# Optimization experiments

Measured on AMD Instinct MI355X. Metric: run time of the kernel, lower is better.

## Reference

```python
import jax, jax.numpy as jnp
import numpy as np


def setup_inputs() -> dict:
    key = jax.random.key(0)
    k1, k2 = jax.random.split(key)
    token_inputs = jax.random.normal(k1, (4, 2048, 4096), dtype=jnp.float32)
    w_gate = jax.random.normal(k2, (4096, 64), dtype=jnp.float32)
    return {"token_inputs": token_inputs, "w_gate": w_gate, "expert_capacity": 40}


def reference(token_inputs, w_gate, expert_capacity):
    # Gating: [b, n, d] @ [d, e] -> [b, n, e]
    router_logits = jnp.einsum('bnd,de->bne', token_inputs, w_gate)

    # Router z-loss: mean of squared logsumexp over experts.
    z_loss = jnp.mean(jax.nn.logsumexp(router_logits, axis=-1) ** 2)

    router_probs = jax.nn.softmax(router_logits, axis=-1)
    num_experts = router_probs.shape[-1]

    # Top-1 (Switch) routing.
    expert_index = jnp.argmax(router_probs, axis=-1)          # [b, n]
    expert_gate = jnp.max(router_probs, axis=-1)              # [b, n]
    expert_mask = jax.nn.one_hot(expert_index, num_experts,
                                 dtype=router_probs.dtype)    # [b, n, e]

    # Load-balancing auxiliary loss.
    density = jnp.mean(expert_mask, axis=1)                   # [b, e] dispatch fraction
    density_proxy = jnp.mean(router_probs, axis=1)            # [b, e] mean prob
    aux_loss = jnp.mean(density * density_proxy) * (num_experts ** 2)

    # Capacity assignment via cumulative sum over tokens (0-based slot index).
    position_in_expert = (jnp.cumsum(expert_mask, axis=1) - 1.0) * expert_mask  # [b, n, e]
    within_capacity = (position_in_expert < expert_capacity).astype(router_probs.dtype) * expert_mask

    pos_idx = position_in_expert.astype(jnp.int32)            # [b, n, e]
    # Dispatch: one-hot over capacity slots, zeroed for dropped tokens. [b, n, e, c]
    dispatch_tensor = within_capacity[..., None] * jax.nn.one_hot(
        pos_idx, expert_capacity, dtype=router_probs.dtype)
    # Combine: dispatch scaled by the router gate probability.
    combine_tensor = dispatch_tensor * expert_gate[:, :, None, None]

    return dispatch_tensor, combine_tensor, aux_loss, z_loss
```

## Files before the change

kernel.cpp:

```cpp
#include <hip/hip_runtime.h>
#include <stdint.h>

#define B_    4
#define N_    2048
#define D_    4096
#define E_    64
#define TOKENS (B_ * N_)
#define KT    16
#define TM    128
#define KS    16
#define KCHUNK (D_ / KS)
#define NIT   (KCHUNK / KT)
#define PA    (TM + 4)
#define PW    (E_ + 4)

typedef float vfloat4 __attribute__((ext_vector_type(4)));

__global__ __launch_bounds__(256) void k_gemm_z(const float* __restrict__ A,
                                                const float* __restrict__ W,
                                                float* __restrict__ P,
                                                float* __restrict__ out,
                                                float* __restrict__ probsum,
                                                float* __restrict__ losses) {
    __shared__ float As[KT][PA];
    __shared__ float Ws[KT][PW];

    const int tid   = threadIdx.x;
    const int tok0  = blockIdx.x * TM;
    const int kc    = blockIdx.y;
    const int kbase = kc * KCHUNK;
    const int blin  = kc * gridDim.x + blockIdx.x;

    const int t0 = (tid & 15) * 8;
    const int e0 = (tid >> 4) * 4;

    const int a_k = (tid & 3) * 4;
    const int a_t = tid >> 2;
    const int w_k = tid >> 4;
    const int w_e = (tid & 15) * 4;

    vfloat4* zbase = reinterpret_cast<vfloat4*>(out) + (size_t)blin * 10240 + tid;
    int zstep = 0;
    const vfloat4 z4 = {0.f, 0.f, 0.f, 0.f};

    if (blin == 0) {
        probsum[tid] = 0.f;
        if (tid < 2) losses[tid] = 0.f;
    }

    const float* gA = A + (size_t)tok0 * D_ + kbase;

    float4 pa0 = *reinterpret_cast<const float4*>(gA + (size_t)a_t * D_ + a_k);
    float4 pa1 = *reinterpret_cast<const float4*>(gA + (size_t)(a_t + 64) * D_ + a_k);
    float4 pw  = *reinterpret_cast<const float4*>(W + (size_t)(kbase + w_k) * E_ + w_e);

    float acc[8][4] = {{0.f}};

    #pragma unroll 1
    for (int it = 0; it < NIT; ++it) {
        As[a_k + 0][a_t]      = pa0.x;
        As[a_k + 1][a_t]      = pa0.y;
        As[a_k + 2][a_t]      = pa0.z;
        As[a_k + 3][a_t]      = pa0.w;
        As[a_k + 0][a_t + 64] = pa1.x;
        As[a_k + 1][a_t + 64] = pa1.y;
        As[a_k + 2][a_t + 64] = pa1.z;
        As[a_k + 3][a_t + 64] = pa1.w;
        *reinterpret_cast<float4*>(&Ws[w_k][w_e]) = pw;
        __syncthreads();

        if (it + 1 < NIT) {
            const int ko = (it + 1) * KT;
            pa0 = *reinterpret_cast<const float4*>(gA + (size_t)a_t * D_ + ko + a_k);
            pa1 = *reinterpret_cast<const float4*>(gA + (size_t)(a_t + 64) * D_ + ko + a_k);
            pw  = *reinterpret_cast<const float4*>(W + (size_t)(kbase + ko + w_k) * E_ + w_e);
        }

        {
            const int nz = (it < 8) ? 3 : 2;
            for (int j = 0; j < nz; ++j) {
                __builtin_nontemporal_store(z4, zbase + (size_t)zstep * 256);
                ++zstep;
            }
        }

        #pragma unroll
        for (int kk = 0; kk < KT; ++kk) {
            float a[8], b[4];
            *reinterpret_cast<float4*>(&a[0]) = *reinterpret_cast<const float4*>(&As[kk][t0]);
            *reinterpret_cast<float4*>(&a[4]) = *reinterpret_cast<const float4*>(&As[kk][t0 + 4]);
            *reinterpret_cast<float4*>(&b[0]) = *reinterpret_cast<const float4*>(&Ws[kk][e0]);
            #pragma unroll
            for (int i = 0; i < 8; ++i)
                #pragma unroll
                for (int j = 0; j < 4; ++j)
                    acc[i][j] += a[i] * b[j];
        }
        __syncthreads();
    }

    float* base = P + ((size_t)kc * TOKENS + tok0) * E_;
    #pragma unroll
    for (int i = 0; i < 8; ++i) {
        const float4 v = make_float4(acc[i][0], acc[i][1], acc[i][2], acc[i][3]);
        *reinterpret_cast<float4*>(&base[(size_t)(t0 + i) * E_ + e0]) = v;
    }
}

__global__ __launch_bounds__(256) void k_softmax(const float* __restrict__ P,
                                                 int* __restrict__ idx,
                                                 float* __restrict__ gate,
                                                 float* __restrict__ probsum,
                                                 float* __restrict__ out_z) {
    const int tid  = threadIdx.x;
    const int wid  = tid >> 6;
    const int lane = tid & 63;
    const int tok  = blockIdx.x * 4 + wid;

    float l = 0.f;
    #pragma unroll
    for (int kc = 0; kc < KS; ++kc)
        l += P[((size_t)kc * TOKENS + tok) * E_ + lane];

    float m = l; int mi = lane;
    #pragma unroll
    for (int off = 32; off > 0; off >>= 1) {
        const float om = __shfl_down(m, off);
        const int   oi = __shfl_down(mi, off);
        if (om > m || (om == m && oi < mi)) { m = om; mi = oi; }
    }
    m  = __shfl(m, 0);
    mi = __shfl(mi, 0);

    const float p = __expf(l - m);
    float s = p;
    #pragma unroll
    for (int off = 32; off > 0; off >>= 1) s += __shfl_down(s, off);
    s = __shfl(s, 0);

    __shared__ float pacc[4][E_];
    __shared__ float zv[4];
    pacc[wid][lane] = p / s;
    if (lane == 0) {
        const float lse = m + logf(s);
        zv[wid]   = lse * lse;
        idx[tok]  = mi;
        gate[tok] = 1.0f / s;
    }
    __syncthreads();

    if (tid < E_) {
        const float ps = pacc[0][tid] + pacc[1][tid] + pacc[2][tid] + pacc[3][tid];
        const int b = (blockIdx.x * 4) / N_;
        atomicAdd(&probsum[b * E_ + tid], ps);
    }
    if (tid == 0)
        atomicAdd(out_z, (zv[0] + zv[1] + zv[2] + zv[3]) * (1.0f / (float)TOKENS));
}

__global__ __launch_bounds__(64) void k_posloss(const int* __restrict__ idx,
                                                const float* __restrict__ gate,
                                                const float* __restrict__ probsum,
                                                float* __restrict__ out,
                                                float* __restrict__ out_aux,
                                                int C, size_t half) {
    const int b = blockIdx.x >> 6;
    const int e = blockIdx.x & 63;
    const int lane = threadIdx.x;
    const int*   ib = idx  + b * N_;
    const float* gb = gate + b * N_;
    float* ob = out + (size_t)b * N_ * E_ * C;

    int running = 0;
    for (int step = 0; step < N_ / 64; ++step) {
        const int t = step * 64 + lane;
        const bool match = (ib[t] == e);
        const unsigned long long mask = __ballot(match);
        if (match) {
            const int p = running + __popcll(mask & ((1ull << lane) - 1ull));
            if (p < C) {
                const size_t off = (size_t)t * E_ * C + (size_t)e * C + p;
                ob[off] = 1.0f;
                ob[half + off] = gb[t];
            }
        }
        running += __popcll(mask);
    }
    if (lane == 0)
        atomicAdd(out_aux,
                  (float)running * probsum[b * E_ + e] * (1.0f / 262144.0f));
}

extern "C" void kernel_launch(void* const* d_in, const int* in_sizes, int n_in,
                              void* d_out, int out_size, void* d_ws, size_t ws_size,
                              hipStream_t stream) {
    const float* A = (const float*)d_in[0];
    const float* W = (const float*)d_in[1];
    float* out = (float*)d_out;

    const size_t half = ((size_t)out_size - 2) / 2;
    const int C = (int)(half / ((size_t)TOKENS * E_));

    float* P = (float*)d_ws;
    size_t off = (size_t)KS * TOKENS * E_;
    int*   idx     = (int*)(P + off);   off += TOKENS;
    float* gate    = P + off;           off += TOKENS;
    float* probsum = P + off;           off += B_ * E_;

    float* out_aux = out + 2 * half;
    float* out_z   = out + 2 * half + 1;

    k_gemm_z<<<dim3(TOKENS / TM, KS), 256, 0, stream>>>(A, W, P, out, probsum,
                                                        out_aux);
    k_softmax<<<TOKENS / 4, 256, 0, stream>>>(P, idx, gate, probsum, out_z);
    k_posloss<<<B_ * E_, 64, 0, stream>>>(idx, gate, probsum, out, out_aux, C, half);
}
```

Baseline: 339.0 us.

## Split output zero-fill into dedicated blocks and transpose GEMM thread tile

The zero-fill of the large dispatch/combine output moves out of the GEMM main loop into 256 dedicated fill blocks launched in the same 1D grid, with the GEMM blocks re-indexed after them. The per-thread GEMM micro-tile also changes from 8 tokens x 4 experts to 4 tokens x 8 experts, which alters the LDS read pattern. The aim is to stop interleaving stores with the compute loop so fill and GEMM blocks run concurrently. The trade-off is that fill blocks are scheduled first and may delay GEMM blocks. Correctness relies on qsteps dividing the output size exactly.

```diff
diff --git a/kernel.cpp b/kernel.cpp
--- a/kernel.cpp
+++ b/kernel.cpp
@@ -13,6 +13,8 @@
 #define NIT   (KCHUNK / KT)
 #define PA    (TM + 4)
 #define PW    (E_ + 4)
+#define FILLB 256
+#define GEMMB ((TOKENS / TM) * KS)
 
 typedef float vfloat4 __attribute__((ext_vector_type(4)));
 
@@ -21,40 +23,46 @@
                                                 float* __restrict__ P,
                                                 float* __restrict__ out,
                                                 float* __restrict__ probsum,
-                                                float* __restrict__ losses) {
+                                                float* __restrict__ losses,
+                                                int qsteps) {
+    const int tid = threadIdx.x;
+
+    if (blockIdx.x < FILLB) {
+        vfloat4* zb = reinterpret_cast<vfloat4*>(out)
+                    + (size_t)blockIdx.x * (size_t)qsteps * 256 + tid;
+        const vfloat4 z4 = {0.f, 0.f, 0.f, 0.f};
+        for (int s = 0; s < qsteps; ++s)
+            __builtin_nontemporal_store(z4, zb + (size_t)s * 256);
+        if (blockIdx.x == 0) {
+            probsum[tid] = 0.f;
+            if (tid < 2) losses[tid] = 0.f;
+        }
+        return;
+    }
+
     __shared__ float As[KT][PA];
     __shared__ float Ws[KT][PW];
 
-    const int tid   = threadIdx.x;
-    const int tok0  = blockIdx.x * TM;
-    const int kc    = blockIdx.y;
+    const int bid   = blockIdx.x - FILLB;
+    const int tok0  = (bid & 63) * TM;
+    const int kc    = bid >> 6;
     const int kbase = kc * KCHUNK;
-    const int blin  = kc * gridDim.x + blockIdx.x;
-
-    const int t0 = (tid & 15) * 8;
-    const int e0 = (tid >> 4) * 4;
+
+    const int t0 = (tid & 31) * 4;
+    const int e0 = (tid >> 5) * 8;
 
     const int a_k = (tid & 3) * 4;
     const int a_t = tid >> 2;
     const int w_k = tid >> 4;
     const int w_e = (tid & 15) * 4;
 
-    vfloat4* zbase = reinterpret_cast<vfloat4*>(out) + (size_t)blin * 10240 + tid;
-    int zstep = 0;
-    const vfloat4 z4 = {0.f, 0.f, 0.f, 0.f};
-
-    if (blin == 0) {
-        probsum[tid] = 0.f;
-        if (tid < 2) losses[tid] = 0.f;
-    }
-
     const float* gA = A + (size_t)tok0 * D_ + kbase;
 
     float4 pa0 = *reinterpret_cast<const float4*>(gA + (size_t)a_t * D_ + a_k);
     float4 pa1 = *reinterpret_cast<const float4*>(gA + (size_t)(a_t + 64) * D_ + a_k);
     float4 pw  = *reinterpret_cast<const float4*>(W + (size_t)(kbase + w_k) * E_ + w_e);
 
-    float acc[8][4] = {{0.f}};
+    float acc[4][8] = {{0.f}};
 
     #pragma unroll 1
     for (int it = 0; it < NIT; ++it) {
@@ -76,24 +84,16 @@
             pw  = *reinterpret_cast<const float4*>(W + (size_t)(kbase + ko + w_k) * E_ + w_e);
         }
 
-        {
-            const int nz = (it < 8) ? 3 : 2;
-            for (int j = 0; j < nz; ++j) {
-                __builtin_nontemporal_store(z4, zbase + (size_t)zstep * 256);
-                ++zstep;
-            }
-        }
-
         #pragma unroll
         for (int kk = 0; kk < KT; ++kk) {
-            float a[8], b[4];
+            float a[4], b[8];
             *reinterpret_cast<float4*>(&a[0]) = *reinterpret_cast<const float4*>(&As[kk][t0]);
-            *reinterpret_cast<float4*>(&a[4]) = *reinterpret_cast<const float4*>(&As[kk][t0 + 4]);
             *reinterpret_cast<float4*>(&b[0]) = *reinterpret_cast<const float4*>(&Ws[kk][e0]);
+            *reinterpret_cast<float4*>(&b[4]) = *reinterpret_cast<const float4*>(&Ws[kk][e0 + 4]);
             #pragma unroll
-            for (int i = 0; i < 8; ++i)
+            for (int i = 0; i < 4; ++i)
                 #pragma unroll
-                for (int j = 0; j < 4; ++j)
+                for (int j = 0; j < 8; ++j)
                     acc[i][j] += a[i] * b[j];
         }
         __syncthreads();
@@ -101,9 +101,10 @@
 
     float* base = P + ((size_t)kc * TOKENS + tok0) * E_;
     #pragma unroll
-    for (int i = 0; i < 8; ++i) {
-        const float4 v = make_float4(acc[i][0], acc[i][1], acc[i][2], acc[i][3]);
-        *reinterpret_cast<float4*>(&base[(size_t)(t0 + i) * E_ + e0]) = v;
+    for (int i = 0; i < 4; ++i) {
+        float* row = &base[(size_t)(t0 + i) * E_ + e0];
+        *reinterpret_cast<float4*>(row)     = make_float4(acc[i][0], acc[i][1], acc[i][2], acc[i][3]);
+        *reinterpret_cast<float4*>(row + 4) = make_float4(acc[i][4], acc[i][5], acc[i][6], acc[i][7]);
     }
 }
 
@@ -200,6 +201,7 @@
 
     const size_t half = ((size_t)out_size - 2) / 2;
     const int C = (int)(half / ((size_t)TOKENS * E_));
+    const int qsteps = (int)((2 * half / 4) / ((size_t)FILLB * 256));
 
     float* P = (float*)d_ws;
     size_t off = (size_t)KS * TOKENS * E_;
@@ -210,8 +212,8 @@
     float* out_aux = out + 2 * half;
     float* out_z   = out + 2 * half + 1;
 
-    k_gemm_z<<<dim3(TOKENS / TM, KS), 256, 0, stream>>>(A, W, P, out, probsum,
-                                                        out_aux);
+    k_gemm_z<<<FILLB + GEMMB, 256, 0, stream>>>(A, W, P, out, probsum,
+                                                out_aux, qsteps);
     k_softmax<<<TOKENS / 4, 256, 0, stream>>>(P, idx, gate, probsum, out_z);
     k_posloss<<<B_ * E_, 64, 0, stream>>>(idx, gate, probsum, out, out_aux, C, half);
 }
```

After: 353.0 us. 4.1% more time.
